# Optimization experiments

Hardware: AMD Instinct MI355X
Metric: run time of the kernel (lower is better)

Reference implementation:

```python
import jax, jax.numpy as jnp
import numpy as np

E, D, H, R = 8, 2048, 8192, 64   # experts, d_model(in=out), hidden, rank
N = 4096                          # tokens (batch*seq)


def setup_inputs() -> dict:
    key = jax.random.key(0)
    ks = jax.random.split(key, 8)
    f32 = jnp.float32
    x = jax.random.normal(ks[0], (N, D), f32)
    # Stacked low-rank expert params: expert i = relu(x@u1@v1+b1) @ u2 @ v2 + b2
    u1 = jax.random.normal(ks[1], (E, D, R), f32) / np.float32(np.sqrt(D))
    v1 = jax.random.normal(ks[2], (E, R, H), f32) / np.float32(np.sqrt(R))
    b1 = jnp.zeros((E, H), f32)
    u2 = jax.random.normal(ks[3], (E, H, R), f32) / np.float32(np.sqrt(H))
    v2 = jax.random.normal(ks[4], (E, R, D), f32) / np.float32(np.sqrt(R))
    b2 = jnp.zeros((E, D), f32)
    # gate = nn.Linear(D, E): weight [E, D], bias [E]
    gate_w = jax.random.normal(ks[5], (E, D), f32) / np.float32(np.sqrt(D))
    gate_b = jnp.zeros((E,), f32)
    return dict(x=x, u1=u1, v1=v1, b1=b1, u2=u2, v2=v2, b2=b2,
                gate_w=gate_w, gate_b=gate_b)


def reference(x, u1, v1, b1, u2, v2, b2, gate_w, gate_b):
    # --- routing: softmax gate, top-2, renormalize ---
    logits = x @ gate_w.T + gate_b                      # [N, E]
    probs = jax.nn.softmax(logits, axis=-1)
    top_p, top_i = jax.lax.top_k(probs, 2)              # [N, 2]
    top_p = top_p / jnp.sum(top_p, axis=-1, keepdims=True)
    # combine weight per (token, expert): zero unless expert in top-2
    w = jnp.sum(jax.nn.one_hot(top_i, E, dtype=x.dtype) * top_p[..., None], axis=1)  # [N, E]

    # --- experts: low-rank MLP applied per expert, weighted accumulate ---
    def body(acc, params):
        u1e, v1e, b1e, u2e, v2e, b2e, we = params       # we: [N]
        h = jax.nn.relu((x @ u1e) @ v1e + b1e)          # [N, H]
        y = (h @ u2e) @ v2e + b2e                       # [N, D]
        return acc + we[:, None] * y, None

    out, _ = jax.lax.scan(body, jnp.zeros_like(x), (u1, v1, b1, u2, v2, b2, w.T))
    return out
```

## Files before the change

### kernel.cpp

```cpp
#include <hip/hip_runtime.h>
#include <hip/hip_bf16.h>

#define E 8
#define D 2048
#define H 8192
#define R 64
#define NTOK 4096
#define HSPLIT 4
#define HPER (H / HSPLIT)
#define MSLOT 128

typedef __attribute__((ext_vector_type(8))) short bf16x8;
typedef __attribute__((ext_vector_type(4))) float f32x4;
typedef __attribute__((ext_vector_type(16))) float f32x16;

__device__ __forceinline__ unsigned short f2b(float f){
  union { __hip_bfloat16 h; unsigned short u; } cv;
  cv.h = __float2bfloat16(f);
  return cv.u;
}
__device__ __forceinline__ float b2f(unsigned short u){
  union { unsigned int i; float f; } cv; cv.i = ((unsigned int)u) << 16; return cv.f;
}

__device__ __forceinline__ bf16x8 ldfrag(const unsigned short* base, int row0, int k0,
                                         int pitch, int lane){
  return *reinterpret_cast<const bf16x8*>(base + (row0 + (lane & 15)) * pitch
                                          + k0 + ((lane >> 4) << 3));
}
__device__ __forceinline__ bf16x8 ldfrag32(const unsigned short* base, int row0, int k0,
                                           int pitch, int lane){
  return *reinterpret_cast<const bf16x8*>(base + (row0 + (lane & 31)) * pitch
                                          + k0 + ((lane >> 5) << 3));
}

__global__ __launch_bounds__(256) void pack_tr(const float* __restrict__ src,
                                               unsigned short* __restrict__ dst,
                                               int RS, int CS){
  int e = blockIdx.z;
  const float* s = src + (size_t)e * RS * CS;
  unsigned short* d = dst + (size_t)e * RS * CS;
  int c0 = blockIdx.x * 64, r0 = blockIdx.y * 64;
  int l = threadIdx.x & 63, cb = (threadIdx.x >> 6) * 16;
  int r = r0 + l;
  const float4* sp = reinterpret_cast<const float4*>(s + (size_t)r * CS + c0 + cb);
  float v[16];
  #pragma unroll
  for (int q = 0; q < 4; ++q){
    float4 t = sp[q];
    v[q*4] = t.x; v[q*4+1] = t.y; v[q*4+2] = t.z; v[q*4+3] = t.w;
  }
  #pragma unroll
  for (int j = 0; j < 16; ++j)
    d[(size_t)(c0 + cb + j) * RS + r] = f2b(v[j]);
}

__global__ __launch_bounds__(256) void gate_kernel(
    const float* __restrict__ x, const float* __restrict__ gw,
    const float* __restrict__ gb, int* __restrict__ tsl,
    unsigned short* __restrict__ xb)
{
  int wid  = threadIdx.x >> 6;
  int lane = threadIdx.x & 63;
  int n0 = blockIdx.x * 8 + wid * 2;

  float acc[2][E];
  #pragma unroll
  for (int t = 0; t < 2; ++t)
    #pragma unroll
    for (int e = 0; e < E; ++e) acc[t][e] = 0.f;

  for (int i = 0; i < D / 256; ++i){
    int dd = i * 256 + lane * 4;
    float4 xv[2];
    #pragma unroll
    for (int t = 0; t < 2; ++t){
      xv[t] = *reinterpret_cast<const float4*>(x + (size_t)(n0 + t) * D + dd);
      unsigned short o[4] = { f2b(xv[t].x), f2b(xv[t].y), f2b(xv[t].z), f2b(xv[t].w) };
      *reinterpret_cast<ushort4*>(xb + (size_t)(n0 + t) * D + dd) = *reinterpret_cast<ushort4*>(o);
    }
    #pragma unroll
    for (int e = 0; e < E; ++e){
      float4 g = *reinterpret_cast<const float4*>(gw + (size_t)e * D + dd);
      #pragma unroll
      for (int t = 0; t < 2; ++t)
        acc[t][e] += xv[t].x * g.x + xv[t].y * g.y + xv[t].z * g.z + xv[t].w * g.w;
    }
  }

  #pragma unroll
  for (int t = 0; t < 2; ++t){
    #pragma unroll
    for (int e = 0; e < E; ++e){
      float v = acc[t][e];
      for (int off = 32; off; off >>= 1) v += __shfl_xor(v, off, 64);
      acc[t][e] = v + gb[e];
    }
    if (lane == 0){
      int n = n0 + t;
      float l0 = -1e30f, l1 = -1e30f; int i0 = 0, i1 = 0;
      #pragma unroll
      for (int e = 0; e < E; ++e){
        float v = acc[t][e];
        if (v > l0){ l1 = l0; i1 = i0; l0 = v; i0 = e; }
        else if (v > l1){ l1 = v; i1 = e; }
      }
      float tt = expf(l1 - l0);
      float w0 = 1.f / (1.f + tt);
      float w1 = tt * w0;
      int* ts = tsl + n * 8;
      ts[0] = i0; ts[2] = __float_as_int(w0);
      ts[3] = i1; ts[5] = __float_as_int(w1);
    }
  }
}

__global__ __launch_bounds__(256) void route_kernel(
    int* __restrict__ tsl, int* __restrict__ cnt, int* __restrict__ lst)
{
  int wid  = threadIdx.x >> 6;
  int lane = threadIdx.x & 63;
  int tok  = blockIdx.x * 256 + wid * 64 + lane;
  int* ts = tsl + tok * 8;
  int i0 = ts[0], i1 = ts[3];
  unsigned long long below = (1ULL << lane) - 1ULL;

  #pragma unroll
  for (int e = 0; e < E; ++e){
    unsigned long long m0 = __ballot(i0 == e);
    unsigned long long m1 = __ballot(i1 == e);
    int c0  = __popcll(m0);
    int tot = c0 + __popcll(m1);
    int base = 0;
    if (lane == 0 && tot) base = atomicAdd(&cnt[e], tot);
    base = __shfl(base, 0, 64);
    if (i0 == e){
      int p = base + __popcll(m0 & below);
      lst[e * NTOK + p] = tok;  ts[1] = p;
    }
    if (i1 == e){
      int p = base + c0 + __popcll(m1 & below);
      lst[e * NTOK + p] = tok;  ts[4] = p;
    }
  }
}

__global__ __launch_bounds__(256) void t1_kernel(
    const unsigned short* __restrict__ xb, const unsigned short* __restrict__ u1p,
    const int* __restrict__ cnt, const int* __restrict__ lst,
    unsigned short* __restrict__ T1buf)
{
  int e = blockIdx.y;
  int nc = cnt[e];
  int t0 = blockIdx.x * 64;
  if (t0 >= nc) return;

  __shared__ int s_tok[64];
  __shared__ unsigned short Xs[64 * 136];
  __shared__ unsigned short U1s[64 * 136];
  int tid = threadIdx.x, w = tid >> 6, lane = tid & 63;

  if (tid < 64) s_tok[tid] = lst[e * NTOK + min(t0 + tid, nc - 1)];
  __syncthreads();

  int m = (w & 3) * 16;
  f32x4 z = {0.f, 0.f, 0.f, 0.f};
  f32x4 acc[4] = {z, z, z, z};

  for (int kc = 0; kc < D; kc += 128){
    __syncthreads();
    #pragma unroll
    for (int s = 0; s < 4; ++s){
      int id = tid + s * 256;
      int rr = id >> 4, c = (id & 15) * 8;
      *reinterpret_cast<bf16x8*>(&Xs[rr * 136 + c]) =
        *reinterpret_cast<const bf16x8*>(&xb[(size_t)s_tok[rr] * D + kc + c]);
      *reinterpret_cast<bf16x8*>(&U1s[rr * 136 + c]) =
        *reinterpret_cast<const bf16x8*>(&u1p[((size_t)e * R + rr) * D + kc + c]);
    }
    __syncthreads();
    #pragma unroll
    for (int j = 0; j < 4; ++j)
      #pragma unroll
      for (int ks = 0; ks < 4; ++ks)
        acc[j] = __builtin_amdgcn_mfma_f32_16x16x32_bf16(
            ldfrag(Xs, m, ks * 32, 136, lane),
            ldfrag(U1s, j * 16, ks * 32, 136, lane), acc[j], 0, 0, 0);
  }
  #pragma unroll
  for (int j = 0; j < 4; ++j){
    int col = j * 16 + (lane & 15);
    #pragma unroll
    for (int q = 0; q < 4; ++q){
      int row = m + ((lane >> 4) << 2) + q;
      T1buf[((size_t)e * NTOK + t0 + row) * R + col] = f2b(acc[j][q]);
    }
  }
}

__global__ __launch_bounds__(512, 2) void mid_kernel(
    const unsigned short* __restrict__ T1buf, const unsigned short* __restrict__ v1p,
    const unsigned short* __restrict__ u2p, const float* __restrict__ b1,
    const int* __restrict__ cnt, float* __restrict__ T2acc)
{
  int e = blockIdx.z;
  int nc = cnt[e];
  int t0 = blockIdx.x * MSLOT;
  if (t0 >= nc) return;
  int hc0 = blockIdx.y * HPER;

  __shared__ unsigned short T1s[MSLOT * 72];
  __shared__ unsigned short v1s[128 * 72];
  __shared__ unsigned short u2s[64 * 136];
  __shared__ unsigned short Hs[MSLOT * 136];
  __shared__ float b1s[HPER];

  int tid = threadIdx.x, w = tid >> 6, lane = tid & 63;

  #pragma unroll
  for (int s = 0; s < 2; ++s){
    int id = tid + s * 512;
    int rr = id >> 3, c = (id & 7) * 8;
    *reinterpret_cast<bf16x8*>(&T1s[rr * 72 + c]) =
      *reinterpret_cast<const bf16x8*>(&T1buf[((size_t)e * NTOK + t0 + rr) * R + c]);
  }
  for (int i = tid; i < HPER; i += 512) b1s[i] = b1[(size_t)e * H + hc0 + i];

  int mB = (w & 3) * 32;
  int nB = (w >> 2) * 64;
  int kh = (w >> 2) * 64;

  f32x16 acc0, acc1;
  #pragma unroll
  for (int q = 0; q < 16; ++q){ acc0[q] = 0.f; acc1[q] = 0.f; }

  bf16x8 pv[2], pu[2];
  #pragma unroll
  for (int s = 0; s < 2; ++s){
    int id = tid + s * 512;
    pv[s] = *reinterpret_cast<const bf16x8*>(&v1p[((size_t)e * H + hc0 + (id >> 3)) * R + (id & 7) * 8]);
    pu[s] = *reinterpret_cast<const bf16x8*>(&u2p[((size_t)e * R + (id >> 4)) * H + hc0 + (id & 15) * 8]);
  }

  for (int hs = 0; hs < HPER; hs += 128){
    __syncthreads();
    #pragma unroll
    for (int s = 0; s < 2; ++s){
      int id = tid + s * 512;
      *reinterpret_cast<bf16x8*>(&v1s[(id >> 3) * 72 + (id & 7) * 8]) = pv[s];
      *reinterpret_cast<bf16x8*>(&u2s[(id >> 4) * 136 + (id & 15) * 8]) = pu[s];
    }
    __syncthreads();

    f32x16 h0, h1;
    #pragma unroll
    for (int q = 0; q < 16; ++q){ h0[q] = 0.f; h1[q] = 0.f; }
    #pragma unroll
    for (int kc = 0; kc < 4; ++kc){
      bf16x8 a = ldfrag32(T1s, mB, kc * 16, 72, lane);
      h0 = __builtin_amdgcn_mfma_f32_32x32x16_bf16(
          a, ldfrag32(v1s, nB, kc * 16, 72, lane), h0, 0, 0, 0);
      h1 = __builtin_amdgcn_mfma_f32_32x32x16_bf16(
          a, ldfrag32(v1s, nB + 32, kc * 16, 72, lane), h1, 0, 0, 0);
    }
    {
      int c0 = nB + (lane & 31);
      float bv0 = b1s[hs + c0], bv1 = b1s[hs + c0 + 32];
      #pragma unroll
      for (int q = 0; q < 16; ++q){
        int srow = mB + (q & 3) + 8 * (q >> 2) + 4 * (lane >> 5);
        float v0 = h0[q] + bv0, v1v = h1[q] + bv1;
        Hs[srow * 136 + c0]      = f2b(v0 > 0.f ? v0 : 0.f);
        Hs[srow * 136 + c0 + 32] = f2b(v1v > 0.f ? v1v : 0.f);
      }
    }
    int hn = (hs + 128 < HPER) ? hs + 128 : 0;
    #pragma unroll
    for (int s = 0; s < 2; ++s){
      int id = tid + s * 512;
      pv[s] = *reinterpret_cast<const bf16x8*>(&v1p[((size_t)e * H + hc0 + hn + (id >> 3)) * R + (id & 7) * 8]);
      pu[s] = *reinterpret_cast<const bf16x8*>(&u2p[((size_t)e * R + (id >> 4)) * H + hc0 + hn + (id & 15) * 8]);
    }
    __syncthreads();

    #pragma unroll
    for (int kc = 0; kc < 4; ++kc){
      bf16x8 a = ldfrag32(Hs, mB, kh + kc * 16, 136, lane);
      acc0 = __builtin_amdgcn_mfma_f32_32x32x16_bf16(
          a, ldfrag32(u2s, 0,  kh + kc * 16, 136, lane), acc0, 0, 0, 0);
      acc1 = __builtin_amdgcn_mfma_f32_32x32x16_bf16(
          a, ldfrag32(u2s, 32, kh + kc * 16, 136, lane), acc1, 0, 0, 0);
    }
  }

  int col = lane & 31;
  #pragma unroll
  for (int q = 0; q < 16; ++q){
    int srow = mB + (q & 3) + 8 * (q >> 2) + 4 * (lane >> 5);
    float* dst = &T2acc[((size_t)e * NTOK + t0 + srow) * R];
    atomicAdd(dst + col,      acc0[q]);
    atomicAdd(dst + col + 32, acc1[q]);
  }
}

__global__ __launch_bounds__(512, 4) void out_kernel(
    const float* __restrict__ T2acc, const unsigned short* __restrict__ v2p,
    const float* __restrict__ b2, const int* __restrict__ cnt,
    unsigned short* __restrict__ yb)
{
  int e = blockIdx.y;
  int nc = cnt[e];
  int t0 = blockIdx.x * 64;
  if (t0 >= nc) return;
  int base = 0;
  #pragma unroll
  for (int i = 0; i < E; ++i) base += (i < e) ? cnt[i] : 0;

  __shared__ unsigned short T2s[64 * 72];
  __shared__ unsigned short v2s[256 * 72];
  __shared__ float b2s[D];
  int tid = threadIdx.x, w = tid >> 6, lane = tid & 63;

  { int rr = tid >> 3, c = (tid & 7) * 8;
    const float* src = &T2acc[((size_t)e * NTOK + t0 + rr) * R + c];
    float4 a = *reinterpret_cast<const float4*>(src);
    float4 b = *reinterpret_cast<const float4*>(src + 4);
    unsigned short o[8] = { f2b(a.x), f2b(a.y), f2b(a.z), f2b(a.w),
                            f2b(b.x), f2b(b.y), f2b(b.z), f2b(b.w) };
    *reinterpret_cast<bf16x8*>(&T2s[rr * 72 + c]) = *reinterpret_cast<bf16x8*>(o); }
  for (int i = tid; i < D; i += 512) b2s[i] = b2[(size_t)e * D + i];

  int m1 = (w & 1) * 32, nb = (w >> 1) * 64;
  f32x4 z = {0.f, 0.f, 0.f, 0.f};

  for (int dc = 0; dc < D; dc += 256){
    __syncthreads();
    #pragma unroll
    for (int s = 0; s < 4; ++s){
      int id = tid + s * 512;
      int rr = id >> 3, c = (id & 7) * 8;
      *reinterpret_cast<bf16x8*>(&v2s[rr * 72 + c]) =
        *reinterpret_cast<const bf16x8*>(&v2p[((size_t)e * D + dc + rr) * R + c]);
    }
    __syncthreads();
    #pragma unroll
    for (int i = 0; i < 2; ++i)
      #pragma unroll
      for (int j = 0; j < 4; ++j){
        f32x4 a = z;
        #pragma unroll
        for (int ks = 0; ks < 2; ++ks)
          a = __builtin_amdgcn_mfma_f32_16x16x32_bf16(
              ldfrag(T2s, m1 + i * 16, ks * 32, 72, lane),
              ldfrag(v2s, nb + j * 16, ks * 32, 72, lane), a, 0, 0, 0);
        int dcol = dc + nb + j * 16 + (lane & 15);
        float bv = b2s[dcol];
        #pragma unroll
        for (int q = 0; q < 4; ++q){
          int row = m1 + i * 16 + ((lane >> 4) << 2) + q;
          if (t0 + row < nc)
            yb[((size_t)(base + t0 + row)) * D + dcol] = f2b(a[q] + bv);
        }
      }
  }
}

__global__ __launch_bounds__(256) void combine_kernel(
    const unsigned short* __restrict__ yb, const int* __restrict__ tsl,
    const int* __restrict__ cnt, float* __restrict__ out)
{
  int tok = blockIdx.x;
  int d0 = threadIdx.x * 8;
  const int* ts = tsl + tok * 8;
  int e0 = ts[0], p0 = ts[1]; float w0 = __int_as_float(ts[2]);
  int e1 = ts[3], p1 = ts[4]; float w1 = __int_as_float(ts[5]);
  int b0 = 0, b1s = 0;
  #pragma unroll
  for (int i = 0; i < E; ++i){
    int c = cnt[i];
    b0  += (i < e0) ? c : 0;
    b1s += (i < e1) ? c : 0;
  }
  bf16x8 y0 = *reinterpret_cast<const bf16x8*>(&yb[((size_t)(b0 + p0)) * D + d0]);
  bf16x8 y1 = *reinterpret_cast<const bf16x8*>(&yb[((size_t)(b1s + p1)) * D + d0]);
  float o[8];
  #pragma unroll
  for (int j = 0; j < 8; ++j)
    o[j] = w0 * b2f((unsigned short)y0[j]) + w1 * b2f((unsigned short)y1[j]);
  *reinterpret_cast<float4*>(&out[(size_t)tok * D + d0])     = *reinterpret_cast<float4*>(&o[0]);
  *reinterpret_cast<float4*>(&out[(size_t)tok * D + d0 + 4]) = *reinterpret_cast<float4*>(&o[4]);
}

extern "C" void kernel_launch(void* const* d_in, const int* in_sizes, int n_in,
                              void* d_out, int out_size, void* d_ws, size_t ws_size,
                              hipStream_t stream)
{
  const float* x  = (const float*)d_in[0];
  const float* u1 = (const float*)d_in[1];
  const float* v1 = (const float*)d_in[2];
  const float* b1 = (const float*)d_in[3];
  const float* u2 = (const float*)d_in[4];
  const float* v2 = (const float*)d_in[5];
  const float* b2 = (const float*)d_in[6];
  const float* gw = (const float*)d_in[7];
  const float* gb = (const float*)d_in[8];
  float* out = (float*)d_out;

  const size_t SZ_XB  = (size_t)NTOK * D * 2;
  const size_t SZ_U1P = (size_t)E * R * D * 2;
  const size_t SZ_V1P = (size_t)E * H * R * 2;
  const size_t SZ_U2P = (size_t)E * R * H * 2;
  const size_t SZ_V2P = (size_t)E * D * R * 2;
  const size_t SZ_T1  = (size_t)E * NTOK * R * 2;
  const size_t SZ_T2  = (size_t)E * NTOK * R * 4;

  char* ws = (char*)d_ws;
  size_t o = 0;
  auto take = [&](size_t b){ void* p = ws + o; o = (o + b + 255) & ~(size_t)255; return p; };
  int* cnt = (int*)take(E * 4);
  int* lst = (int*)take((size_t)E * NTOK * 4);
  int* tsl = (int*)take((size_t)NTOK * 8 * 4);
  char* A  = (char*)take(SZ_XB + SZ_U1P + SZ_V1P + SZ_U2P);
  unsigned short* xb  = (unsigned short*)A;
  unsigned short* u1p = (unsigned short*)(A + SZ_XB);
  unsigned short* v1p = (unsigned short*)(A + SZ_XB + SZ_U1P);
  unsigned short* u2p = (unsigned short*)(A + SZ_XB + SZ_U1P + SZ_V1P);
  unsigned short* yb  = (unsigned short*)A;
  unsigned short* v2p = (unsigned short*)take(SZ_V2P);
  unsigned short* T1buf = (unsigned short*)take(SZ_T1);
  float* T2acc = (float*)take(SZ_T2);

  hipMemsetAsync(cnt, 0, E * 4, stream);
  hipMemsetAsync(T2acc, 0, SZ_T2, stream);

  gate_kernel<<<NTOK / 8, 256, 0, stream>>>(x, gw, gb, tsl, xb);
  route_kernel<<<NTOK / 256, 256, 0, stream>>>(tsl, cnt, lst);
  pack_tr<<<dim3(1, D / 64, E), 256, 0, stream>>>(u1, u1p, D, R);
  pack_tr<<<dim3(H / 64, 1, E), 256, 0, stream>>>(v1, v1p, R, H);
  pack_tr<<<dim3(1, H / 64, E), 256, 0, stream>>>(u2, u2p, H, R);
  pack_tr<<<dim3(D / 64, 1, E), 256, 0, stream>>>(v2, v2p, R, D);

  t1_kernel<<<dim3(NTOK / 64, E), 256, 0, stream>>>(xb, u1p, cnt, lst, T1buf);
  mid_kernel<<<dim3(NTOK / MSLOT, HSPLIT, E), 512, 0, stream>>>(T1buf, v1p, u2p, b1, cnt, T2acc);
  out_kernel<<<dim3(NTOK / 64, E), 512, 0, stream>>>(T2acc, v2p, b2, cnt, yb);
  combine_kernel<<<NTOK, 256, 0, stream>>>(yb, tsl, cnt, out);
}
```

Measured before the change: 342.7 us.

## Keep T1 fragments in registers, transpose H tile, drop a barrier, split H finer

The mid kernel stops staging the T1 token tile through shared memory. Each wave now holds its 32-token T1 fragments in registers and computes the hidden tile transposed (v1 as the A operand), so it writes H with vectorized 4-wide stores. Because each wave then reads back only the Hs region it wrote itself, the barrier between the H write and the second GEMM is removed. HSPLIT goes from 4 to 8 and occupancy is raised to 4 blocks per CU for more parallelism, at the cost of twice as many atomicAdds into T2acc and more register pressure.

New measurement: 322.8 us. 1.06x faster.

```diff
diff --git a/kernel.cpp b/kernel.cpp
--- a/kernel.cpp
+++ b/kernel.cpp
@@ -6,9 +6,10 @@
 #define H 8192
 #define R 64
 #define NTOK 4096
-#define HSPLIT 4
+#define HSPLIT 8
 #define HPER (H / HSPLIT)
 #define MSLOT 128
+#define SH 128
 
 typedef __attribute__((ext_vector_type(8))) short bf16x8;
 typedef __attribute__((ext_vector_type(4))) float f32x4;
@@ -198,7 +199,7 @@
   }
 }
 
-__global__ __launch_bounds__(512, 2) void mid_kernel(
+__global__ __launch_bounds__(512, 4) void mid_kernel(
     const unsigned short* __restrict__ T1buf, const unsigned short* __restrict__ v1p,
     const unsigned short* __restrict__ u2p, const float* __restrict__ b1,
     const int* __restrict__ cnt, float* __restrict__ T2acc)
@@ -209,26 +210,22 @@
   if (t0 >= nc) return;
   int hc0 = blockIdx.y * HPER;
 
-  __shared__ unsigned short T1s[MSLOT * 72];
-  __shared__ unsigned short v1s[128 * 72];
+  __shared__ unsigned short v1s[SH * 72];
   __shared__ unsigned short u2s[64 * 136];
   __shared__ unsigned short Hs[MSLOT * 136];
   __shared__ float b1s[HPER];
 
   int tid = threadIdx.x, w = tid >> 6, lane = tid & 63;
-
-  #pragma unroll
-  for (int s = 0; s < 2; ++s){
-    int id = tid + s * 512;
-    int rr = id >> 3, c = (id & 7) * 8;
-    *reinterpret_cast<bf16x8*>(&T1s[rr * 72 + c]) =
-      *reinterpret_cast<const bf16x8*>(&T1buf[((size_t)e * NTOK + t0 + rr) * R + c]);
-  }
+  int s0 = (w & 3) * 32;
+  int hb = (w >> 2) * 64;
+
   for (int i = tid; i < HPER; i += 512) b1s[i] = b1[(size_t)e * H + hc0 + i];
 
-  int mB = (w & 3) * 32;
-  int nB = (w >> 2) * 64;
-  int kh = (w >> 2) * 64;
+  bf16x8 t1f[4];
+  #pragma unroll
+  for (int kc = 0; kc < 4; ++kc)
+    t1f[kc] = *reinterpret_cast<const bf16x8*>(
+        &T1buf[((size_t)e * NTOK + t0 + s0 + (lane & 31)) * R + kc * 16 + ((lane >> 5) << 3)]);
 
   f32x16 acc0, acc1;
   #pragma unroll
@@ -242,7 +239,7 @@
     pu[s] = *reinterpret_cast<const bf16x8*>(&u2p[((size_t)e * R + (id >> 4)) * H + hc0 + (id & 15) * 8]);
   }
 
-  for (int hs = 0; hs < HPER; hs += 128){
+  for (int hs = 0; hs < HPER; hs += SH){
     __syncthreads();
     #pragma unroll
     for (int s = 0; s < 2; ++s){
@@ -252,51 +249,52 @@
     }
     __syncthreads();
 
-    f32x16 h0, h1;
-    #pragma unroll
-    for (int q = 0; q < 16; ++q){ h0[q] = 0.f; h1[q] = 0.f; }
-    #pragma unroll
-    for (int kc = 0; kc < 4; ++kc){
-      bf16x8 a = ldfrag32(T1s, mB, kc * 16, 72, lane);
-      h0 = __builtin_amdgcn_mfma_f32_32x32x16_bf16(
-          a, ldfrag32(v1s, nB, kc * 16, 72, lane), h0, 0, 0, 0);
-      h1 = __builtin_amdgcn_mfma_f32_32x32x16_bf16(
-          a, ldfrag32(v1s, nB + 32, kc * 16, 72, lane), h1, 0, 0, 0);
-    }
-    {
-      int c0 = nB + (lane & 31);
-      float bv0 = b1s[hs + c0], bv1 = b1s[hs + c0 + 32];
-      #pragma unroll
-      for (int q = 0; q < 16; ++q){
-        int srow = mB + (q & 3) + 8 * (q >> 2) + 4 * (lane >> 5);
-        float v0 = h0[q] + bv0, v1v = h1[q] + bv1;
-        Hs[srow * 136 + c0]      = f2b(v0 > 0.f ? v0 : 0.f);
-        Hs[srow * 136 + c0 + 32] = f2b(v1v > 0.f ? v1v : 0.f);
+    int ccol = s0 + (lane & 31);
+    #pragma unroll
+    for (int tile = 0; tile < 2; ++tile){
+      int hT = hb + tile * 32;
+      f32x16 hacc;
+      #pragma unroll
+      for (int q = 0; q < 16; ++q) hacc[q] = 0.f;
+      #pragma unroll
+      for (int kc = 0; kc < 4; ++kc)
+        hacc = __builtin_amdgcn_mfma_f32_32x32x16_bf16(
+            ldfrag32(v1s, hT, kc * 16, 72, lane), t1f[kc], hacc, 0, 0, 0);
+      #pragma unroll
+      for (int g = 0; g < 4; ++g){
+        int hw = hT + 8 * g + 4 * (lane >> 5);
+        unsigned short o[4];
+        #pragma unroll
+        for (int j = 0; j < 4; ++j){
+          float v = hacc[4 * g + j] + b1s[hs + hw + j];
+          o[j] = f2b(v > 0.f ? v : 0.f);
+        }
+        *reinterpret_cast<ushort4*>(&Hs[ccol * 136 + hw]) = *reinterpret_cast<ushort4*>(o);
       }
     }
-    int hn = (hs + 128 < HPER) ? hs + 128 : 0;
+
+    int hn = (hs + SH < HPER) ? hs + SH : 0;
     #pragma unroll
     for (int s = 0; s < 2; ++s){
       int id = tid + s * 512;
       pv[s] = *reinterpret_cast<const bf16x8*>(&v1p[((size_t)e * H + hc0 + hn + (id >> 3)) * R + (id & 7) * 8]);
       pu[s] = *reinterpret_cast<const bf16x8*>(&u2p[((size_t)e * R + (id >> 4)) * H + hc0 + hn + (id & 15) * 8]);
     }
-    __syncthreads();
 
     #pragma unroll
     for (int kc = 0; kc < 4; ++kc){
-      bf16x8 a = ldfrag32(Hs, mB, kh + kc * 16, 136, lane);
+      bf16x8 a = ldfrag32(Hs, s0, hb + kc * 16, 136, lane);
       acc0 = __builtin_amdgcn_mfma_f32_32x32x16_bf16(
-          a, ldfrag32(u2s, 0,  kh + kc * 16, 136, lane), acc0, 0, 0, 0);
+          a, ldfrag32(u2s, 0,  hb + kc * 16, 136, lane), acc0, 0, 0, 0);
       acc1 = __builtin_amdgcn_mfma_f32_32x32x16_bf16(
-          a, ldfrag32(u2s, 32, kh + kc * 16, 136, lane), acc1, 0, 0, 0);
+          a, ldfrag32(u2s, 32, hb + kc * 16, 136, lane), acc1, 0, 0, 0);
     }
   }
 
   int col = lane & 31;
   #pragma unroll
   for (int q = 0; q < 16; ++q){
-    int srow = mB + (q & 3) + 8 * (q >> 2) + 4 * (lane >> 5);
+    int srow = s0 + (q & 3) + 8 * (q >> 2) + 4 * (lane >> 5);
     float* dst = &T2acc[((size_t)e * NTOK + t0 + srow) * R];
     atomicAdd(dst + col,      acc0[q]);
     atomicAdd(dst + col + 32, acc1[q]);
```
